# Kernel optimization log

Measured on AMD Instinct MI355X. Metric: run time of the kernel, lower is better.

Reference implementation:

```python
import jax, jax.numpy as jnp
import numpy as np

N = 50000      # nodes
E = 800000     # edges (avg degree 16)
IN = 128       # in_channels
OUT = 200      # out_channels


def setup_inputs() -> dict:
    key = jax.random.key(0)
    ks = jax.random.split(key, 12)
    x = jax.random.normal(ks[0], (N, IN), dtype=jnp.float32)
    src = jax.random.randint(ks[1], (E,), 0, N, dtype=jnp.int32)
    off = jax.random.randint(ks[2], (E,), 1, N, dtype=jnp.int32)
    dst = (src + off) % N  # guarantees no self-loops (PyG ChebConv removes them)
    edge_index = jnp.stack([src, dst])
    edge_weight = jax.random.uniform(ks[3], (E,), dtype=jnp.float32) + 0.1
    s = 0.05
    # scale_1 (K=1): one weight; scale_2 (K=2): two; scale_3 (K=3): three. Biases per scale.
    return {
        "x": x,
        "edge_index": edge_index,
        "edge_weight": edge_weight,
        "w1_0": jax.random.normal(ks[4], (IN, OUT), dtype=jnp.float32) * s,
        "b1": jnp.zeros((OUT,), dtype=jnp.float32),
        "w2_0": jax.random.normal(ks[5], (IN, OUT), dtype=jnp.float32) * s,
        "w2_1": jax.random.normal(ks[6], (IN, OUT), dtype=jnp.float32) * s,
        "b2": jnp.zeros((OUT,), dtype=jnp.float32),
        "w3_0": jax.random.normal(ks[7], (IN, OUT), dtype=jnp.float32) * s,
        "w3_1": jax.random.normal(ks[8], (IN, OUT), dtype=jnp.float32) * s,
        "w3_2": jax.random.normal(ks[9], (IN, OUT), dtype=jnp.float32) * s,
        "b3": jnp.zeros((OUT,), dtype=jnp.float32),
    }


def _cheb_norm(edge_index, edge_weight, num_nodes):
    # PyG ChebConv.__norm__ with normalization='sym', lambda_max=2.0:
    # L = I - D^{-1/2} A D^{-1/2}; Lhat = 2L/lambda_max - I = -D^{-1/2} A D^{-1/2}
    # (self-loop weights become exactly 0, so we can drop them)
    row, col = edge_index[0], edge_index[1]
    deg = jax.ops.segment_sum(edge_weight, row, num_segments=num_nodes)
    dis = jnp.where(deg > 0, jax.lax.rsqrt(deg), 0.0)
    return -dis[row] * edge_weight * dis[col]


def _propagate(h, src, dst, norm, num_nodes):
    # out[i] = sum_{(j->i) in E} norm_e * h[j]
    return jax.ops.segment_sum(norm[:, None] * h[src], dst, num_segments=num_nodes)


def reference(x, edge_index, edge_weight, w1_0, b1, w2_0, w2_1, b2, w3_0, w3_1, w3_2, b3):
    num_nodes = x.shape[0]
    src, dst = edge_index[0], edge_index[1]
    norm = _cheb_norm(edge_index, edge_weight, num_nodes)
    # Chebyshev recursion (shared across the three scales; identical math):
    tx0 = x                                              # T_0(L) x
    tx1 = _propagate(tx0, src, dst, norm, num_nodes)     # T_1(L) x = Lhat x
    tx2 = 2.0 * _propagate(tx1, src, dst, norm, num_nodes) - tx0  # T_2(L) x
    s1 = tx0 @ w1_0 + b1
    s2 = tx0 @ w2_0 + tx1 @ w2_1 + b2
    s3 = tx0 @ w3_0 + tx1 @ w3_1 + tx2 @ w3_2 + b3
    return (s1, s2, s3)
```

## Files before the change

kernel.cpp:

```cpp
#include <hip/hip_runtime.h>

#define IN 128
#define OUT 200
#define NT 13
#define MT 64
#define RANGES 8
#define REPLICAS 64
#define RBMAX 6272

typedef __bf16 bf16x8 __attribute__((ext_vector_type(8)));
typedef float f32x4 __attribute__((ext_vector_type(4)));
typedef unsigned short ushort;
typedef ushort ushort8 __attribute__((ext_vector_type(8)));
typedef unsigned int uint;

__device__ inline ushort f2bf(float f) {
  uint b = __float_as_uint(f);
  return (ushort)((b + 0x7FFFu + ((b >> 16) & 1u)) >> 16);
}
__device__ inline float bf_lo(uint v) { return __uint_as_float(v << 16); }
__device__ inline float bf_hi(uint v) { return __uint_as_float(v & 0xFFFF0000u); }

__device__ inline size_t pk_idx(int row, int ch) {
  int rt = row >> 4, lr = row & 15, kk = ch >> 5, hi = (ch & 31) >> 3;
  return ((size_t)(rt * 4 + kk) * 64 + hi * 16 + lr) * 8 + (ch & 7);
}

__device__ inline void gload16(const void* g, void* l) {
  __builtin_amdgcn_global_load_lds(
      (const __attribute__((address_space(1))) void*)g,
      (__attribute__((address_space(3))) void*)l, 16, 0, 0);
}


__global__ __launch_bounds__(256) void k_hist(
    const int* __restrict__ src, const int* __restrict__ dst,
    const float* __restrict__ w, float* __restrict__ deg_part,
    int* __restrict__ cnt_part, int E, int N, int RB, int SL) {
  __shared__ float degL[RBMAX];
  __shared__ int cntL[RBMAX];
  int range = blockIdx.x / REPLICAS;
  int rep = blockIdx.x % REPLICAS;
  int base = range * RB;
  int lim = min(N - base, RB);
  for (int i = threadIdx.x; i < RB; i += 256) { degL[i] = 0.f; cntL[i] = 0; }
  __syncthreads();
  int e0 = rep * SL, e1 = min(E, e0 + SL);
  for (int e = e0 + (int)threadIdx.x; e < e1; e += 256) {
    int s = src[e], d = dst[e];
    int sl = s - base, dl = d - base;
    if ((unsigned)sl < (unsigned)lim) atomicAdd(&degL[sl], w[e]);
    if ((unsigned)dl < (unsigned)lim) atomicAdd(&cntL[dl], 1);
  }
  __syncthreads();
  for (int i = threadIdx.x; i < lim; i += 256) {
    deg_part[(size_t)rep * N + base + i] = degL[i];
    cnt_part[(size_t)rep * N + base + i] = cntL[i];
  }
}

__global__ void k_dis_scan(const float* __restrict__ deg_part, int* __restrict__ cnt_part,
                           float* __restrict__ dis,
                           int* __restrict__ offs, int* __restrict__ bsum, int n) {
  __shared__ int s[256];
  int t = threadIdx.x;
  int i = blockIdx.x * 256 + t;
  int v = 0;
  if (i < n) {
    float d = 0.f;
    int run = 0;
    for (int c = 0; c < REPLICAS; ++c) {
      size_t idx = (size_t)c * n + i;
      int cv = cnt_part[idx];
      cnt_part[idx] = run;
      run += cv;
      d += deg_part[idx];
    }
    v = run;
    dis[i] = d > 0.f ? rsqrtf(d) : 0.f;
  }
  s[t] = v;
  __syncthreads();
  for (int o = 1; o < 256; o <<= 1) {
    int a = (t >= o) ? s[t - o] : 0;
    __syncthreads();
    s[t] += a;
    __syncthreads();
  }
  if (i < n) offs[i] = s[t] - v;
  if (t == 255) bsum[blockIdx.x] = s[255];
}

__global__ void k_scan_c2(int* __restrict__ offs, const int* __restrict__ bsum,
                          int n, int E) {
  __shared__ int red[256];
  int t = threadIdx.x;
  int partial = 0;
  for (int i = t; i < (int)blockIdx.x; i += 256) partial += bsum[i];
  red[t] = partial;
  __syncthreads();
  for (int o = 128; o > 0; o >>= 1) {
    if (t < o) red[t] += red[t + o];
    __syncthreads();
  }
  int base = red[0];
  int i = blockIdx.x * 256 + t;
  if (i < n) offs[i] += base;
  if (i == 0) offs[n] = E;
}

__global__ __launch_bounds__(256) void k_fill(
    const int* __restrict__ src, const int* __restrict__ dst,
    const float* __restrict__ w, const float* __restrict__ dis,
    const int* __restrict__ offs, const int* __restrict__ pref,
    int2* __restrict__ csr_rec, int E, int N, int RB, int SL) {
  __shared__ int curL[RBMAX];
  int range = blockIdx.x / REPLICAS;
  int rep = blockIdx.x % REPLICAS;
  int base = range * RB;
  int lim = min(N - base, RB);
  for (int i = threadIdx.x; i < RB; i += 256) curL[i] = 0;
  __syncthreads();
  int e0 = rep * SL, e1 = min(E, e0 + SL);
  for (int e = e0 + (int)threadIdx.x; e < e1; e += 256) {
    int d = dst[e];
    int dl = d - base;
    if ((unsigned)dl < (unsigned)lim) {
      int s = src[e];
      int r = atomicAdd(&curL[dl], 1);
      int pos = offs[d] + pref[(size_t)rep * N + d] + r;
      float nm = -dis[s] * w[e] * dis[d];
      csr_rec[pos] = make_int2(s, __float_as_int(nm));
    }
  }
}


__global__ void k_cast_pack(const float* __restrict__ x, ushort* __restrict__ xb,
                            ushort* __restrict__ xp, int cast_blocks, long totx,
                            const float* __restrict__ w10, const float* __restrict__ w20,
                            const float* __restrict__ w21, const float* __restrict__ w30,
                            const float* __restrict__ w31, const float* __restrict__ w32,
                            ushort* __restrict__ wpack) {
  if (blockIdx.x < (unsigned)cast_blocks) {
    long i = ((long)blockIdx.x * blockDim.x + threadIdx.x) * 8;
    if (i >= totx) return;
    float4 a = *(const float4*)&x[i];
    float4 b = *(const float4*)&x[i + 4];
    ushort8 o;
    o[0] = f2bf(a.x); o[1] = f2bf(a.y); o[2] = f2bf(a.z); o[3] = f2bf(a.w);
    o[4] = f2bf(b.x); o[5] = f2bf(b.y); o[6] = f2bf(b.z); o[7] = f2bf(b.w);
    *(ushort8*)&xb[i] = o;
    int row = (int)(i >> 7), ch = (int)(i & 127);
    *(ushort8*)&xp[pk_idx(row, ch)] = o;
  } else {
    int gid = (blockIdx.x - cast_blocks) * blockDim.x + threadIdx.x;
    int total = 6 * NT * 4 * 64;
    if (gid >= total) return;
    int lane = gid & 63;
    int f = gid >> 6;
    int kk = f & 3;
    int g2 = f >> 2;
    int m = g2 % 6;
    int t = g2 / 6;
    const float* w = (m == 0) ? w10 : (m == 1) ? w20 : (m == 2) ? w21
                   : (m == 3) ? w30 : (m == 4) ? w31 : w32;
    int col = t * 16 + (lane & 15);
    int kbase = kk * 32 + (lane >> 4) * 8;
    ushort8 o;
#pragma unroll
    for (int j = 0; j < 8; ++j)
      o[j] = (col < OUT) ? f2bf(w[(kbase + j) * OUT + col]) : (ushort)0;
    *(ushort8*)&wpack[(size_t)gid * 8] = o;
  }
}


template <int MODE>
__global__ void k_gather(const ushort* __restrict__ h, const ushort* __restrict__ xb,
                         const int2* __restrict__ csr_rec,
                         const int* __restrict__ offs, ushort* __restrict__ out_lin,
                         ushort* __restrict__ out_pk, int n) {
  int node = blockIdx.x * 4 + (threadIdx.x >> 6);
  if (node >= n) return;
  int lane = threadIdx.x & 63;
  int ch0 = lane * 2;
  int s = offs[node], e = offs[node + 1];
  float lo[8], hi[8];
#pragma unroll
  for (int q = 0; q < 8; ++q) { lo[q] = 0.f; hi[q] = 0.f; }
  int p = s;
  for (; p + 7 < e; p += 8) {
    int2 rec[8]; uint v[8];
#pragma unroll
    for (int q = 0; q < 8; ++q) rec[q] = csr_rec[p + q];
#pragma unroll
    for (int q = 0; q < 8; ++q) v[q] = *(const uint*)&h[(size_t)rec[q].x * IN + ch0];
#pragma unroll
    for (int q = 0; q < 8; ++q) {
      float nm = __int_as_float(rec[q].y);
      lo[q] = fmaf(nm, bf_lo(v[q]), lo[q]);
      hi[q] = fmaf(nm, bf_hi(v[q]), hi[q]);
    }
  }
  for (; p + 1 < e; p += 2) {
    int2 r0 = csr_rec[p], r1 = csr_rec[p + 1];
    uint v0 = *(const uint*)&h[(size_t)r0.x * IN + ch0];
    uint v1 = *(const uint*)&h[(size_t)r1.x * IN + ch0];
    float n0 = __int_as_float(r0.y), n1 = __int_as_float(r1.y);
    lo[0] = fmaf(n0, bf_lo(v0), lo[0]); hi[0] = fmaf(n0, bf_hi(v0), hi[0]);
    lo[1] = fmaf(n1, bf_lo(v1), lo[1]); hi[1] = fmaf(n1, bf_hi(v1), hi[1]);
  }
  if (p < e) {
    int2 r0 = csr_rec[p];
    float n0 = __int_as_float(r0.y);
    uint v0 = *(const uint*)&h[(size_t)r0.x * IN + ch0];
    lo[2] = fmaf(n0, bf_lo(v0), lo[2]); hi[2] = fmaf(n0, bf_hi(v0), hi[2]);
  }
  float r0 = ((lo[0] + lo[1]) + (lo[2] + lo[3])) + ((lo[4] + lo[5]) + (lo[6] + lo[7]));
  float r1 = ((hi[0] + hi[1]) + (hi[2] + hi[3])) + ((hi[4] + hi[5]) + (hi[6] + hi[7]));
  if (MODE == 1) {
    uint xv = *(const uint*)&xb[(size_t)node * IN + ch0];
    r0 = 2.f * r0 - bf_lo(xv);
    r1 = 2.f * r1 - bf_hi(xv);
  }
  uint packed = (uint)f2bf(r0) | ((uint)f2bf(r1) << 16);
  if (MODE == 0)
    *(uint*)&out_lin[(size_t)node * IN + ch0] = packed;
  *(uint*)&out_pk[pk_idx(node, ch0)] = packed;
}


__global__ __launch_bounds__(256) void k_gemm_mfma(
    const ushort* __restrict__ xp, const ushort* __restrict__ t1p, const ushort* __restrict__ t2p,
    const ushort* __restrict__ wpack,
    const float* __restrict__ b1v, const float* __restrict__ b2v, const float* __restrict__ b3v,
    float* __restrict__ out, int n) {
  __shared__ ushort bsm[2][24 * 512];
  int lane = threadIdx.x & 63;
  int wave = threadIdx.x >> 6;
  int row0 = blockIdx.x * MT + wave * 16;
  int rt = row0 >> 4;

  bf16x8 a[3][4];
  const ushort* mats[3] = {xp, t1p, t2p};
#pragma unroll
  for (int m = 0; m < 3; ++m) {
#pragma unroll
    for (int kk = 0; kk < 4; ++kk) {
      size_t fi = ((size_t)rt * 4 + kk) * 512 + (size_t)lane * 8;
      a[m][kk] = __builtin_bit_cast(bf16x8, *(const ushort8*)&mats[m][fi]);
    }
  }
#pragma unroll
  for (int m = 0; m < 3; ++m)
#pragma unroll
    for (int kk = 0; kk < 4; ++kk)
      asm volatile("" : "+v"(a[m][kk]));

  long NS = (long)n * OUT;
  float* out1 = out;
  float* out2 = out + NS;
  float* out3 = out + 2 * NS;

  auto stage = [&](int t, int buf) {
    const ushort* src = wpack + (size_t)t * 24 * 512;
#pragma unroll
    for (int j = 0; j < 6; ++j) {
      int c = wave * 6 + j;
      gload16(src + (size_t)c * 512 + (size_t)lane * 8, &bsm[buf][c * 512]);
    }
  };

  stage(0, 0);
  __syncthreads();
  int cur = 0;

  for (int t = 0; t < NT; ++t) {
    if (t + 1 < NT) stage(t + 1, cur ^ 1);

    int col = t * 16 + (lane & 15);
    bool colok = col < OUT;
    int colc = colok ? col : 0;
    float bb1 = colok ? b1v[colc] : 0.f;
    float bb2 = colok ? b2v[colc] : 0.f;
    float bb3 = colok ? b3v[colc] : 0.f;
    f32x4 c1 = {bb1, bb1, bb1, bb1};
    f32x4 c2 = {bb2, bb2, bb2, bb2};
    f32x4 c3 = {bb3, bb3, bb3, bb3};

    const ushort* bb = &bsm[cur][0];
#pragma unroll
    for (int kk = 0; kk < 4; ++kk) {
      bf16x8 b10 = __builtin_bit_cast(bf16x8, *(const ushort8*)&bb[(0 * 4 + kk) * 512 + lane * 8]);
      bf16x8 b20 = __builtin_bit_cast(bf16x8, *(const ushort8*)&bb[(1 * 4 + kk) * 512 + lane * 8]);
      bf16x8 b21 = __builtin_bit_cast(bf16x8, *(const ushort8*)&bb[(2 * 4 + kk) * 512 + lane * 8]);
      bf16x8 b30 = __builtin_bit_cast(bf16x8, *(const ushort8*)&bb[(3 * 4 + kk) * 512 + lane * 8]);
      bf16x8 b31 = __builtin_bit_cast(bf16x8, *(const ushort8*)&bb[(4 * 4 + kk) * 512 + lane * 8]);
      bf16x8 b32 = __builtin_bit_cast(bf16x8, *(const ushort8*)&bb[(5 * 4 + kk) * 512 + lane * 8]);
      c1 = __builtin_amdgcn_mfma_f32_16x16x32_bf16(a[0][kk], b10, c1, 0, 0, 0);
      c2 = __builtin_amdgcn_mfma_f32_16x16x32_bf16(a[0][kk], b20, c2, 0, 0, 0);
      c2 = __builtin_amdgcn_mfma_f32_16x16x32_bf16(a[1][kk], b21, c2, 0, 0, 0);
      c3 = __builtin_amdgcn_mfma_f32_16x16x32_bf16(a[0][kk], b30, c3, 0, 0, 0);
      c3 = __builtin_amdgcn_mfma_f32_16x16x32_bf16(a[1][kk], b31, c3, 0, 0, 0);
      c3 = __builtin_amdgcn_mfma_f32_16x16x32_bf16(a[2][kk], b32, c3, 0, 0, 0);
    }

    if (colok) {
      int rbase = row0 + (lane >> 4) * 4;
#pragma unroll
      for (int r = 0; r < 4; ++r) {
        int ra = rbase + r;
        if (ra < n) {
          out1[(long)ra * OUT + col] = c1[r];
          out2[(long)ra * OUT + col] = c2[r];
          out3[(long)ra * OUT + col] = c3[r];
        }
      }
    }

    __syncthreads();
    cur ^= 1;
  }
}


extern "C" void kernel_launch(void* const* d_in, const int* in_sizes, int n_in,
                              void* d_out, int out_size, void* d_ws, size_t ws_size,
                              hipStream_t stream) {
  const float* x   = (const float*)d_in[0];
  const int*   ei  = (const int*)d_in[1];
  const float* ew  = (const float*)d_in[2];
  const float* w10 = (const float*)d_in[3];
  const float* b1  = (const float*)d_in[4];
  const float* w20 = (const float*)d_in[5];
  const float* w21 = (const float*)d_in[6];
  const float* b2  = (const float*)d_in[7];
  const float* w30 = (const float*)d_in[8];
  const float* w31 = (const float*)d_in[9];
  const float* w32 = (const float*)d_in[10];
  const float* b3  = (const float*)d_in[11];
  float* out = (float*)d_out;

  int N = in_sizes[0] / IN;
  int E = in_sizes[2];
  const int* src = ei;
  const int* dst = ei + E;

  int mtiles = (N + MT - 1) / MT;
  size_t prow = (size_t)mtiles * MT;
  size_t pksz = prow * IN * 2;

  int RB = (N + RANGES - 1) / RANGES;
  int SL = (E + REPLICAS - 1) / REPLICAS;

  char* ws = (char*)d_ws;
  size_t off = 0;
  auto alloc = [&](size_t bytes) {
    void* p = ws + off;
    off = (off + bytes + 15) & ~(size_t)15;
    return p;
  };
  float* deg_part = (float*)alloc((size_t)REPLICAS * N * 4);
  int*   cnt_part = (int*)alloc((size_t)REPLICAS * N * 4);
  float* dis      = (float*)alloc((size_t)N * 4);
  int*   offs     = (int*)alloc(((size_t)N + 1) * 4);
  int2*  csr_rec  = (int2*)alloc((size_t)E * 8);
  int*   bsum     = (int*)alloc(256 * 4);
  ushort* xb      = (ushort*)alloc((size_t)N * IN * 2);
  ushort* tx1b    = (ushort*)alloc((size_t)N * IN * 2);
  ushort* xp      = (ushort*)alloc(pksz);
  ushort* t1p     = (ushort*)alloc(pksz);
  ushort* t2p     = (ushort*)alloc(pksz);
  ushort* wpack   = (ushort*)alloc((size_t)6 * NT * 4 * 64 * 8 * 2);

  const int tb = 256;
  int nb = (N + 255) / 256;

  long totx = (long)N * IN;
  int cast_blocks = (int)((totx / 8 + tb - 1) / tb);
  int wp_blocks = (6 * NT * 4 * 64 + tb - 1) / tb;

  k_hist<<<RANGES * REPLICAS, 256, 0, stream>>>(src, dst, ew, deg_part, cnt_part, E, N, RB, SL);
  k_dis_scan<<<nb, 256, 0, stream>>>(deg_part, cnt_part, dis, offs, bsum, N);
  k_scan_c2<<<nb, 256, 0, stream>>>(offs, bsum, N, E);
  k_fill<<<RANGES * REPLICAS, 256, 0, stream>>>(src, dst, ew, dis, offs, cnt_part, csr_rec, E, N, RB, SL);
  k_cast_pack<<<cast_blocks + wp_blocks, tb, 0, stream>>>(
      x, xb, xp, cast_blocks, totx, w10, w20, w21, w30, w31, w32, wpack);

  int gblk = (N + 3) / 4;
  k_gather<0><<<gblk, 256, 0, stream>>>(xb, xb, csr_rec, offs, tx1b, t1p, N);
  k_gather<1><<<gblk, 256, 0, stream>>>(tx1b, xb, csr_rec, offs, nullptr, t2p, N);

  k_gemm_mfma<<<mtiles, 256, 0, stream>>>(xp, t1p, t2p, wpack, b1, b2, b3, out, N);
}
```

Measured before the change: 238.1 us.

## Split gather channels across grid.y and parallelize edges within wave; relax GEMM barrier waits

The gather kernel now splits the 128 channels into four 32-channel slices via blockIdx.y. Within each wave, four groups of 16 lanes handle different edges in parallel, and the partial sums are combined with cross-lane shuffles. This gives more memory-level parallelism and more waves for the latency-bound neighbor gather. The cost is four times as many reads of the CSR records and 64-byte rather than 256-byte row segments per load. Separately, the GEMM replaces __syncthreads with an explicit vmcnt(12) wait plus s_barrier, so the prefetch of the next weight tile can stay in flight across the barrier.

```diff
diff --git a/kernel.cpp b/kernel.cpp
--- a/kernel.cpp
+++ b/kernel.cpp
@@ -177,57 +177,46 @@
 
 
 template <int MODE>
-__global__ void k_gather(const ushort* __restrict__ h, const ushort* __restrict__ xb,
-                         const int2* __restrict__ csr_rec,
-                         const int* __restrict__ offs, ushort* __restrict__ out_lin,
-                         ushort* __restrict__ out_pk, int n) {
+__global__ __launch_bounds__(256) void k_gather(
+    const ushort* __restrict__ h, const ushort* __restrict__ xb,
+    const int2* __restrict__ csr_rec, const int* __restrict__ offs,
+    ushort* __restrict__ out_lin, ushort* __restrict__ out_pk, int n) {
   int node = blockIdx.x * 4 + (threadIdx.x >> 6);
   if (node >= n) return;
   int lane = threadIdx.x & 63;
-  int ch0 = lane * 2;
+  int eg = lane >> 4;
+  int ch = blockIdx.y * 32 + (lane & 15) * 2;
   int s = offs[node], e = offs[node + 1];
-  float lo[8], hi[8];
-#pragma unroll
-  for (int q = 0; q < 8; ++q) { lo[q] = 0.f; hi[q] = 0.f; }
-  int p = s;
-  for (; p + 7 < e; p += 8) {
-    int2 rec[8]; uint v[8];
-#pragma unroll
-    for (int q = 0; q < 8; ++q) rec[q] = csr_rec[p + q];
-#pragma unroll
-    for (int q = 0; q < 8; ++q) v[q] = *(const uint*)&h[(size_t)rec[q].x * IN + ch0];
-#pragma unroll
-    for (int q = 0; q < 8; ++q) {
-      float nm = __int_as_float(rec[q].y);
-      lo[q] = fmaf(nm, bf_lo(v[q]), lo[q]);
-      hi[q] = fmaf(nm, bf_hi(v[q]), hi[q]);
-    }
-  }
-  for (; p + 1 < e; p += 2) {
-    int2 r0 = csr_rec[p], r1 = csr_rec[p + 1];
-    uint v0 = *(const uint*)&h[(size_t)r0.x * IN + ch0];
-    uint v1 = *(const uint*)&h[(size_t)r1.x * IN + ch0];
-    float n0 = __int_as_float(r0.y), n1 = __int_as_float(r1.y);
-    lo[0] = fmaf(n0, bf_lo(v0), lo[0]); hi[0] = fmaf(n0, bf_hi(v0), hi[0]);
-    lo[1] = fmaf(n1, bf_lo(v1), lo[1]); hi[1] = fmaf(n1, bf_hi(v1), hi[1]);
-  }
-  if (p < e) {
-    int2 r0 = csr_rec[p];
-    float n0 = __int_as_float(r0.y);
-    uint v0 = *(const uint*)&h[(size_t)r0.x * IN + ch0];
-    lo[2] = fmaf(n0, bf_lo(v0), lo[2]); hi[2] = fmaf(n0, bf_hi(v0), hi[2]);
-  }
-  float r0 = ((lo[0] + lo[1]) + (lo[2] + lo[3])) + ((lo[4] + lo[5]) + (lo[6] + lo[7]));
-  float r1 = ((hi[0] + hi[1]) + (hi[2] + hi[3])) + ((hi[4] + hi[5]) + (hi[6] + hi[7]));
-  if (MODE == 1) {
-    uint xv = *(const uint*)&xb[(size_t)node * IN + ch0];
-    r0 = 2.f * r0 - bf_lo(xv);
-    r1 = 2.f * r1 - bf_hi(xv);
-  }
-  uint packed = (uint)f2bf(r0) | ((uint)f2bf(r1) << 16);
-  if (MODE == 0)
-    *(uint*)&out_lin[(size_t)node * IN + ch0] = packed;
-  *(uint*)&out_pk[pk_idx(node, ch0)] = packed;
+  float lo0 = 0.f, hi0 = 0.f, lo1 = 0.f, hi1 = 0.f;
+  for (int p0 = s; p0 < e; p0 += 8) {
+    int p1 = p0 + eg, p2 = p0 + 4 + eg;
+    if (p1 < e) {
+      int2 r = csr_rec[p1];
+      uint v = *(const uint*)&h[(size_t)r.x * IN + ch];
+      float nm = __int_as_float(r.y);
+      lo0 = fmaf(nm, bf_lo(v), lo0); hi0 = fmaf(nm, bf_hi(v), hi0);
+    }
+    if (p2 < e) {
+      int2 r = csr_rec[p2];
+      uint v = *(const uint*)&h[(size_t)r.x * IN + ch];
+      float nm = __int_as_float(r.y);
+      lo1 = fmaf(nm, bf_lo(v), lo1); hi1 = fmaf(nm, bf_hi(v), hi1);
+    }
+  }
+  float r0 = lo0 + lo1, r1 = hi0 + hi1;
+  r0 += __shfl_xor(r0, 16); r1 += __shfl_xor(r1, 16);
+  r0 += __shfl_xor(r0, 32); r1 += __shfl_xor(r1, 32);
+  if (lane < 16) {
+    if (MODE == 1) {
+      uint xv = *(const uint*)&xb[(size_t)node * IN + ch];
+      r0 = 2.f * r0 - bf_lo(xv);
+      r1 = 2.f * r1 - bf_hi(xv);
+    }
+    uint packed = (uint)f2bf(r0) | ((uint)f2bf(r1) << 16);
+    if (MODE == 0)
+      *(uint*)&out_lin[(size_t)node * IN + ch] = packed;
+    *(uint*)&out_pk[pk_idx(node, ch)] = packed;
+  }
 }
 
 
@@ -273,7 +262,8 @@
   };
 
   stage(0, 0);
-  __syncthreads();
+  asm volatile("s_waitcnt vmcnt(0)" ::: "memory");
+  __builtin_amdgcn_s_barrier();
   int cur = 0;
 
   for (int t = 0; t < NT; ++t) {
@@ -319,7 +309,8 @@
       }
     }
 
-    __syncthreads();
+    asm volatile("s_waitcnt vmcnt(12)" ::: "memory");
+    __builtin_amdgcn_s_barrier();
     cur ^= 1;
   }
 }
@@ -388,9 +379,9 @@
   k_cast_pack<<<cast_blocks + wp_blocks, tb, 0, stream>>>(
       x, xb, xp, cast_blocks, totx, w10, w20, w21, w30, w31, w32, wpack);
 
-  int gblk = (N + 3) / 4;
-  k_gather<0><<<gblk, 256, 0, stream>>>(xb, xb, csr_rec, offs, tx1b, t1p, N);
-  k_gather<1><<<gblk, 256, 0, stream>>>(tx1b, xb, csr_rec, offs, nullptr, t2p, N);
+  dim3 gg((N + 3) / 4, 4);
+  k_gather<0><<<gg, 256, 0, stream>>>(xb, xb, csr_rec, offs, tx1b, t1p, N);
+  k_gather<1><<<gg, 256, 0, stream>>>(tx1b, xb, csr_rec, offs, nullptr, t2p, N);
 
   k_gemm_mfma<<<mtiles, 256, 0, stream>>>(xp, t1p, t2p, wpack, b1, b2, b3, out, N);
 }
```

After: 378.4 us. +59.0%, slower.

## Stage GEMM output through LDS for coalesced float4 stores and relax barriers

Applied to the files above, without the earlier changes.

Each wave now writes its MFMA accumulator tiles for two adjacent 16-column tiles into a per-wave LDS staging buffer. It then emits coalesced float4 row stores to the three outputs instead of scattered scalar 4-byte stores. The __syncthreads calls are replaced by explicit s_waitcnt vmcnt plus s_barrier, so that outstanding output stores need not fully drain each iteration. This adds LDS usage and relies on hand-written vmcnt counts being correct for the async weight-tile loads, which risks subtle races.

```diff
diff --git a/kernel.cpp b/kernel.cpp
--- a/kernel.cpp
+++ b/kernel.cpp
@@ -237,6 +237,7 @@
     const float* __restrict__ b1v, const float* __restrict__ b2v, const float* __restrict__ b3v,
     float* __restrict__ out, int n) {
   __shared__ ushort bsm[2][24 * 512];
+  __shared__ float st[4][16][100];
   int lane = threadIdx.x & 63;
   int wave = threadIdx.x >> 6;
   int row0 = blockIdx.x * MT + wave * 16;
@@ -259,9 +260,7 @@
       asm volatile("" : "+v"(a[m][kk]));
 
   long NS = (long)n * OUT;
-  float* out1 = out;
-  float* out2 = out + NS;
-  float* out3 = out + 2 * NS;
+  float* outp[3] = {out, out + NS, out + 2 * NS};
 
   auto stage = [&](int t, int buf) {
     const ushort* src = wpack + (size_t)t * 24 * 512;
@@ -273,7 +272,8 @@
   };
 
   stage(0, 0);
-  __syncthreads();
+  asm volatile("s_waitcnt vmcnt(0)" ::: "memory");
+  __builtin_amdgcn_s_barrier();
   int cur = 0;
 
   for (int t = 0; t < NT; ++t) {
@@ -306,20 +306,48 @@
       c3 = __builtin_amdgcn_mfma_f32_16x16x32_bf16(a[2][kk], b32, c3, 0, 0, 0);
     }
 
-    if (colok) {
-      int rbase = row0 + (lane >> 4) * 4;
+    if (t < NT - 1) {
+      int rloc = (lane >> 4) * 4;
+      int cloc = (t & 1) * 16 + (lane & 15);
 #pragma unroll
       for (int r = 0; r < 4; ++r) {
-        int ra = rbase + r;
-        if (ra < n) {
-          out1[(long)ra * OUT + col] = c1[r];
-          out2[(long)ra * OUT + col] = c2[r];
-          out3[(long)ra * OUT + col] = c3[r];
+        st[wave][rloc + r][cloc]      = c1[r];
+        st[wave][rloc + r][32 + cloc] = c2[r];
+        st[wave][rloc + r][64 + cloc] = c3[r];
+      }
+      if (t & 1) {
+        int tp = t >> 1;
+        int col0 = tp * 32 + (lane & 7) * 4;
+#pragma unroll
+        for (int m = 0; m < 3; ++m) {
+#pragma unroll
+          for (int hb = 0; hb < 2; ++hb) {
+            int row = hb * 8 + (lane >> 3);
+            int ra = row0 + row;
+            float4 v = *(const float4*)&st[wave][row][m * 32 + (lane & 7) * 4];
+            if (ra < n) *(float4*)&outp[m][(long)ra * OUT + col0] = v;
+          }
+        }
+        asm volatile("s_waitcnt vmcnt(6)" ::: "memory");
+      } else {
+        asm volatile("s_waitcnt vmcnt(0)" ::: "memory");
+      }
+    } else {
+      if (colok) {
+        int rbase = row0 + (lane >> 4) * 4;
+#pragma unroll
+        for (int r = 0; r < 4; ++r) {
+          int ra = rbase + r;
+          if (ra < n) {
+            outp[0][(long)ra * OUT + col] = c1[r];
+            outp[1][(long)ra * OUT + col] = c2[r];
+            outp[2][(long)ra * OUT + col] = c3[r];
+          }
         }
       }
-    }
-
-    __syncthreads();
+      asm volatile("s_waitcnt vmcnt(0)" ::: "memory");
+    }
+    __builtin_amdgcn_s_barrier();
     cur ^= 1;
   }
 }
```

Measured after the change: 241.2 us. Within noise of the previous version (+1.3%).

## Split GEMM into per-output passes and stage results through LDS for coalesced stores

Applied to the files above, without the earlier changes.

The fused three-output GEMM loop becomes three templated passes, one per scale. Each pass accumulates all 13 column tiles in registers, then writes them to a shared-memory staging tile and stores full rows as float4 vectors. The old code wrote scattered 4-byte stores per lane; the new store pattern is meant to be coalesced. In exchange the weight tiles are streamed three times, each pass adds barriers, and the 53KB staging buffer may lower occupancy.

```diff
diff --git a/kernel.cpp b/kernel.cpp
--- a/kernel.cpp
+++ b/kernel.cpp
@@ -231,16 +231,80 @@
 }
 
 
+template <int NM, int CH0>
+__device__ __forceinline__ void gemm_pass(
+    const bf16x8 (&a)[3][4], const ushort* __restrict__ wpack,
+    ushort (&bsm)[2][12 * 512], float (&st)[MT][212],
+    const float* __restrict__ bias, float* __restrict__ outm,
+    int n, int lane, int wave, int blk) {
+  auto stage = [&](int t, int buf) {
+    const ushort* src = wpack + ((size_t)t * 24 + CH0) * 512;
+#pragma unroll
+    for (int j = 0; j < NM; ++j) {
+      int c = wave * NM + j;
+      gload16(src + (size_t)c * 512 + (size_t)lane * 8, &bsm[buf][c * 512]);
+    }
+  };
+  stage(0, 0);
+  asm volatile("s_waitcnt vmcnt(0)" ::: "memory");
+  __builtin_amdgcn_s_barrier();
+
+  f32x4 acc[NT];
+#pragma unroll
+  for (int t = 0; t < NT; ++t) {
+    int col = t * 16 + (lane & 15);
+    float bb = bias[min(col, OUT - 1)];
+    acc[t] = (f32x4){bb, bb, bb, bb};
+  }
+
+  int cur = 0;
+#pragma unroll
+  for (int t = 0; t < NT; ++t) {
+    if (t + 1 < NT) stage(t + 1, cur ^ 1);
+    const ushort* bb_ = &bsm[cur][0];
+#pragma unroll
+    for (int kk = 0; kk < 4; ++kk) {
+#pragma unroll
+      for (int mm = 0; mm < NM; ++mm) {
+        bf16x8 b = __builtin_bit_cast(bf16x8,
+            *(const ushort8*)&bb_[(mm * 4 + kk) * 512 + lane * 8]);
+        acc[t] = __builtin_amdgcn_mfma_f32_16x16x32_bf16(a[mm][kk], b, acc[t], 0, 0, 0);
+      }
+    }
+    asm volatile("s_waitcnt vmcnt(0)" ::: "memory");
+    __builtin_amdgcn_s_barrier();
+    cur ^= 1;
+  }
+
+  int rbase = wave * 16 + (lane >> 4) * 4;
+#pragma unroll
+  for (int t = 0; t < NT; ++t) {
+    int c = t * 16 + (lane & 15);
+#pragma unroll
+    for (int r = 0; r < 4; ++r) st[rbase + r][c] = acc[t][r];
+  }
+#pragma unroll
+  for (int r = 0; r < 16; ++r) {
+    int lrow = wave * 16 + r;
+    long grow = (long)blk * MT + lrow;
+    if (grow < n && lane < 50) {
+      float4 v = *(const float4*)&st[lrow][lane * 4];
+      *(float4*)&outm[grow * OUT + lane * 4] = v;
+    }
+  }
+}
+
 __global__ __launch_bounds__(256) void k_gemm_mfma(
     const ushort* __restrict__ xp, const ushort* __restrict__ t1p, const ushort* __restrict__ t2p,
     const ushort* __restrict__ wpack,
     const float* __restrict__ b1v, const float* __restrict__ b2v, const float* __restrict__ b3v,
     float* __restrict__ out, int n) {
-  __shared__ ushort bsm[2][24 * 512];
+  __shared__ ushort bsm[2][12 * 512];
+  __shared__ float st[MT][212];
   int lane = threadIdx.x & 63;
   int wave = threadIdx.x >> 6;
-  int row0 = blockIdx.x * MT + wave * 16;
-  int rt = row0 >> 4;
+  int blk = blockIdx.x;
+  int rt = (blk * MT + wave * 16) >> 4;
 
   bf16x8 a[3][4];
   const ushort* mats[3] = {xp, t1p, t2p};
@@ -259,69 +323,9 @@
       asm volatile("" : "+v"(a[m][kk]));
 
   long NS = (long)n * OUT;
-  float* out1 = out;
-  float* out2 = out + NS;
-  float* out3 = out + 2 * NS;
-
-  auto stage = [&](int t, int buf) {
-    const ushort* src = wpack + (size_t)t * 24 * 512;
-#pragma unroll
-    for (int j = 0; j < 6; ++j) {
-      int c = wave * 6 + j;
-      gload16(src + (size_t)c * 512 + (size_t)lane * 8, &bsm[buf][c * 512]);
-    }
-  };
-
-  stage(0, 0);
-  __syncthreads();
-  int cur = 0;
-
-  for (int t = 0; t < NT; ++t) {
-    if (t + 1 < NT) stage(t + 1, cur ^ 1);
-
-    int col = t * 16 + (lane & 15);
-    bool colok = col < OUT;
-    int colc = colok ? col : 0;
-    float bb1 = colok ? b1v[colc] : 0.f;
-    float bb2 = colok ? b2v[colc] : 0.f;
-    float bb3 = colok ? b3v[colc] : 0.f;
-    f32x4 c1 = {bb1, bb1, bb1, bb1};
-    f32x4 c2 = {bb2, bb2, bb2, bb2};
-    f32x4 c3 = {bb3, bb3, bb3, bb3};
-
-    const ushort* bb = &bsm[cur][0];
-#pragma unroll
-    for (int kk = 0; kk < 4; ++kk) {
-      bf16x8 b10 = __builtin_bit_cast(bf16x8, *(const ushort8*)&bb[(0 * 4 + kk) * 512 + lane * 8]);
-      bf16x8 b20 = __builtin_bit_cast(bf16x8, *(const ushort8*)&bb[(1 * 4 + kk) * 512 + lane * 8]);
-      bf16x8 b21 = __builtin_bit_cast(bf16x8, *(const ushort8*)&bb[(2 * 4 + kk) * 512 + lane * 8]);
-      bf16x8 b30 = __builtin_bit_cast(bf16x8, *(const ushort8*)&bb[(3 * 4 + kk) * 512 + lane * 8]);
-      bf16x8 b31 = __builtin_bit_cast(bf16x8, *(const ushort8*)&bb[(4 * 4 + kk) * 512 + lane * 8]);
-      bf16x8 b32 = __builtin_bit_cast(bf16x8, *(const ushort8*)&bb[(5 * 4 + kk) * 512 + lane * 8]);
-      c1 = __builtin_amdgcn_mfma_f32_16x16x32_bf16(a[0][kk], b10, c1, 0, 0, 0);
-      c2 = __builtin_amdgcn_mfma_f32_16x16x32_bf16(a[0][kk], b20, c2, 0, 0, 0);
-      c2 = __builtin_amdgcn_mfma_f32_16x16x32_bf16(a[1][kk], b21, c2, 0, 0, 0);
-      c3 = __builtin_amdgcn_mfma_f32_16x16x32_bf16(a[0][kk], b30, c3, 0, 0, 0);
-      c3 = __builtin_amdgcn_mfma_f32_16x16x32_bf16(a[1][kk], b31, c3, 0, 0, 0);
-      c3 = __builtin_amdgcn_mfma_f32_16x16x32_bf16(a[2][kk], b32, c3, 0, 0, 0);
-    }
-
-    if (colok) {
-      int rbase = row0 + (lane >> 4) * 4;
-#pragma unroll
-      for (int r = 0; r < 4; ++r) {
-        int ra = rbase + r;
-        if (ra < n) {
-          out1[(long)ra * OUT + col] = c1[r];
-          out2[(long)ra * OUT + col] = c2[r];
-          out3[(long)ra * OUT + col] = c3[r];
-        }
-      }
-    }
-
-    __syncthreads();
-    cur ^= 1;
-  }
+  gemm_pass<1, 0>(a, wpack, bsm, st, b1v, out, n, lane, wave, blk);
+  gemm_pass<2, 4>(a, wpack, bsm, st, b2v, out + NS, n, lane, wave, blk);
+  gemm_pass<3, 12>(a, wpack, bsm, st, b3v, out + 2 * NS, n, lane, wave, blk);
 }
 
 
```

Result: slower. 252.1 us (+5.9%).
